# Kernel optimization log

Hardware: AMD Instinct MI355X
Metric: run time of the kernel (lower is better)

The kernel has to match this reference:

```python
import jax, jax.numpy as jnp
import numpy as np

V = 50000   # input_size == output_size (one-hot vocab)
H = 256     # hidden_size
B = 512     # batch_size
L = 1       # num_layers

def setup_inputs() -> dict:
    key = jax.random.key(0)
    ks = jax.random.split(key, 9)
    s = 1.0 / np.sqrt(H)  # torch default uniform(-1/sqrt(H), 1/sqrt(H))
    inp = {
        "input": jax.random.randint(ks[0], (B,), 0, V, dtype=jnp.int64 if jax.config.jax_enable_x64 else jnp.int32),
        "target": jax.random.randint(ks[1], (B,), 0, V, dtype=jnp.int64 if jax.config.jax_enable_x64 else jnp.int32),
        "hidden": jax.random.normal(ks[2], (L, B, H), dtype=jnp.float32),
        "w_ih": jax.random.uniform(ks[3], (3 * H, V), jnp.float32, -s, s),
        "w_hh": jax.random.uniform(ks[4], (3 * H, H), jnp.float32, -s, s),
        "b_ih": jax.random.uniform(ks[5], (3 * H,), jnp.float32, -s, s),
        "b_hh": jax.random.uniform(ks[6], (3 * H,), jnp.float32, -s, s),
        "w_out": jax.random.uniform(ks[7], (V, H), jnp.float32, -s, s),
        "b_out": jax.random.uniform(ks[8], (V,), jnp.float32, -s, s),
    }
    return inp

def reference(input, target, hidden, w_ih, w_hh, b_ih, b_hh, w_out, b_out):
    # one-hot(input) @ w_ih.T is exactly a row-gather from w_ih.T  -> (B, 3H)
    h0 = hidden[0]                              # (B, H), num_layers == 1
    x_proj = w_ih.T[input] + b_ih               # (B, 3H)
    h_proj = h0 @ w_hh.T + b_hh                 # (B, 3H)
    xr, xz, xn = jnp.split(x_proj, 3, axis=-1)
    hr, hz, hn = jnp.split(h_proj, 3, axis=-1)
    r = jax.nn.sigmoid(xr + hr)                 # reset gate
    z = jax.nn.sigmoid(xz + hz)                 # update gate
    n = jnp.tanh(xn + r * hn)                   # candidate
    h1 = (1.0 - z) * n + z * h0                 # (B, H)
    logit = jnp.tanh(h1 @ w_out.T + b_out)      # (B, V)
    return logit, h1[None]                      # (B,V), (1,B,H)
```

## Files before the change

### kernel.cpp

```cpp
#include <hip/hip_runtime.h>
#include <hip/hip_bf16.h>

#define VOCAB 50000
#define HID   256
#define BATCH 512
#define GH    768

typedef __attribute__((ext_vector_type(8))) __bf16 bf16x8;
typedef __attribute__((ext_vector_type(4))) float f32x4;
typedef __attribute__((ext_vector_type(4))) unsigned int u32x4;

union BFrag {
    bf16x8 v;
    u32x4  q;
    __bf16 b[8];
};

__device__ __forceinline__ float fast_sigmoid(float x) {
    return 1.0f / (1.0f + __expf(-x));
}
__device__ __forceinline__ float fast_tanh(float x) {
    return 1.0f - 2.0f / (1.0f + __expf(2.0f * x));
}

__device__ __forceinline__ void cvt8(BFrag& t, f32x4 lo, f32x4 hi) {
    t.b[0] = (__bf16)lo.x; t.b[1] = (__bf16)lo.y;
    t.b[2] = (__bf16)lo.z; t.b[3] = (__bf16)lo.w;
    t.b[4] = (__bf16)hi.x; t.b[5] = (__bf16)hi.y;
    t.b[6] = (__bf16)hi.z; t.b[7] = (__bf16)hi.w;
}

__device__ __forceinline__ void gload_lds16(const void* g, void* l) {
    __builtin_amdgcn_global_load_lds(
        (const __attribute__((address_space(1))) unsigned int*)g,
        (__attribute__((address_space(3))) unsigned int*)l, 16, 0, 0);
}


__global__ __launch_bounds__(256, 4) void gemm_dma(
    const char* __restrict__ Aswz, const float* __restrict__ Bm,
    float* __restrict__ C, const float* __restrict__ bias, int mChunks)
{
    __shared__ char ldsA[2][16384];

    const int tid  = threadIdx.x;
    const int wid  = tid >> 6;
    const int lane = tid & 63;
    const int r    = lane & 15;
    const int g    = lane >> 4;
    const int col  = blockIdx.x * 64 + wid * 16 + r;
    const int bcol = col < VOCAB ? col : (VOCAB - 1);

    BFrag bf[8];
    {
        const f32x4* wrow = reinterpret_cast<const f32x4*>(Bm + (size_t)bcol * 256);
        #pragma unroll
        for (int kk = 0; kk < 8; kk++) {
            f32x4 lo = __builtin_nontemporal_load(&wrow[kk * 8 + g * 2]);
            f32x4 hi = __builtin_nontemporal_load(&wrow[kk * 8 + g * 2 + 1]);
            cvt8(bf[kk], lo, hi);
        }
    }
    #pragma unroll
    for (int kk = 0; kk < 8; kk++)
        asm volatile("" : "+v"(bf[kk].q));
    const float biasv = bias[bcol];

    auto dma = [&](int c, int buf) {
        const char* src = Aswz + (size_t)c * 16384 + wid * 1024 + lane * 16;
        char* dst = &ldsA[buf][wid * 1024];
        #pragma unroll
        for (int i = 0; i < 4; i++)
            gload_lds16(src + i * 4096, dst + i * 4096);
    };

    dma(0, 0);
    asm volatile("s_waitcnt vmcnt(0)" ::: "memory");
    __builtin_amdgcn_s_barrier();

    for (int c = 0; c < mChunks; c++) {
        const int cur = c & 1;
        if (c + 1 < mChunks) dma(c + 1, cur ^ 1);
        __builtin_amdgcn_sched_barrier(0);

        f32x4 acc0 = (f32x4){0.f, 0.f, 0.f, 0.f};
        f32x4 acc1 = (f32x4){0.f, 0.f, 0.f, 0.f};

        #pragma unroll
        for (int kk = 0; kk < 8; kk++) {
            const int s0 = r * 512 + ((((kk << 2) + g) ^ (r & 7)) << 4);
            BFrag a0, a1;
            a0.q = *reinterpret_cast<const u32x4*>(&ldsA[cur][s0]);
            a1.q = *reinterpret_cast<const u32x4*>(&ldsA[cur][s0 + 8192]);
            acc0 = __builtin_amdgcn_mfma_f32_16x16x32_bf16(a0.v, bf[kk].v, acc0, 0, 0, 0);
            acc1 = __builtin_amdgcn_mfma_f32_16x16x32_bf16(a1.v, bf[kk].v, acc1, 0, 0, 0);
        }

        const int rowb = c * 32 + g * 4;
        #pragma unroll
        for (int j = 0; j < 4; j++) {
            float v0 = fast_tanh(acc0[j] + biasv);
            float v1 = fast_tanh(acc1[j] + biasv);
            C[(size_t)(rowb + j) * VOCAB + bcol]      = v0;
            C[(size_t)(rowb + 16 + j) * VOCAB + bcol] = v1;
        }

        if (c + 1 < mChunks) {
            asm volatile("s_waitcnt vmcnt(8)" ::: "memory");
            __builtin_amdgcn_s_barrier();
        }
    }
}

__global__ __launch_bounds__(256, 4) void gemm_h(
    const float* __restrict__ A, const float* __restrict__ Bm,
    float* __restrict__ C)
{
    __shared__ char ldsA[16384];

    const int tid  = threadIdx.x;
    const int wid  = tid >> 6;
    const int lane = tid & 63;
    const int r    = lane & 15;
    const int g    = lane >> 4;
    const int col  = blockIdx.x * 64 + wid * 16 + r;
    const int mbase = blockIdx.y * 32;

    BFrag bf[8];
    {
        const f32x4* wrow = reinterpret_cast<const f32x4*>(Bm + (size_t)col * 256);
        #pragma unroll
        for (int kk = 0; kk < 8; kk++)
            cvt8(bf[kk], wrow[kk * 8 + g * 2], wrow[kk * 8 + g * 2 + 1]);
    }

    {
        const f32x4* src = reinterpret_cast<const f32x4*>(A + (size_t)mbase * 256);
        #pragma unroll
        for (int i = 0; i < 4; i++) {
            int u = tid + i * 256;
            int row = u >> 5, jj = u & 31;
            BFrag t; cvt8(t, src[2 * u], src[2 * u + 1]);
            int byte = row * 512 + ((jj ^ (row & 7)) << 4);
            *reinterpret_cast<u32x4*>(&ldsA[byte]) = t.q;
        }
    }
    __syncthreads();

    f32x4 acc0 = (f32x4){0.f, 0.f, 0.f, 0.f};
    f32x4 acc1 = (f32x4){0.f, 0.f, 0.f, 0.f};
    #pragma unroll
    for (int kk = 0; kk < 8; kk++) {
        const int s0 = r * 512 + ((((kk << 2) + g) ^ (r & 7)) << 4);
        BFrag a0, a1;
        a0.q = *reinterpret_cast<const u32x4*>(&ldsA[s0]);
        a1.q = *reinterpret_cast<const u32x4*>(&ldsA[s0 + 8192]);
        acc0 = __builtin_amdgcn_mfma_f32_16x16x32_bf16(a0.v, bf[kk].v, acc0, 0, 0, 0);
        acc1 = __builtin_amdgcn_mfma_f32_16x16x32_bf16(a1.v, bf[kk].v, acc1, 0, 0, 0);
    }

    const int rowb = mbase + g * 4;
    #pragma unroll
    for (int j = 0; j < 4; j++) {
        C[(size_t)(rowb + j) * GH + col]      = acc0[j];
        C[(size_t)(rowb + 16 + j) * GH + col] = acc1[j];
    }
}

__global__ __launch_bounds__(256) void gru_gate(
    const int* __restrict__ inp, const float* __restrict__ hidden,
    const float* __restrict__ w_ih, const float* __restrict__ b_ih,
    const float* __restrict__ b_hh, const float* __restrict__ hproj,
    float* __restrict__ h1out, char* __restrict__ h1swz)
{
    const int b = blockIdx.x;
    const int k = threadIdx.x;
    const int c = inp[b];

    float xr = w_ih[(size_t)k * VOCAB + c]         + b_ih[k];
    float xz = w_ih[(size_t)(k + 256) * VOCAB + c] + b_ih[k + 256];
    float xn = w_ih[(size_t)(k + 512) * VOCAB + c] + b_ih[k + 512];

    float hr = hproj[b * GH + k]       + b_hh[k];
    float hz = hproj[b * GH + 256 + k] + b_hh[k + 256];
    float hn = hproj[b * GH + 512 + k] + b_hh[k + 512];

    float rg = fast_sigmoid(xr + hr);
    float zg = fast_sigmoid(xz + hz);
    float ng = fast_tanh(xn + rg * hn);
    float h0 = hidden[b * HID + k];
    float h1 = (1.0f - zg) * ng + zg * h0;

    h1out[b * HID + k] = h1;

    const int row = b & 31, j = k >> 3, e = k & 7;
    size_t byte = (size_t)(b >> 5) * 16384 + row * 512
                + ((j ^ (row & 7)) << 4) + e * 2;
    __bf16 hb = (__bf16)h1;
    *reinterpret_cast<unsigned short*>(h1swz + byte) =
        __builtin_bit_cast(unsigned short, hb);
}

extern "C" void kernel_launch(void* const* d_in, const int* in_sizes, int n_in,
                              void* d_out, int out_size, void* d_ws, size_t ws_size,
                              hipStream_t stream) {
    const int*   input  = (const int*)  d_in[0];
    const float* hidden = (const float*)d_in[2];
    const float* w_ih   = (const float*)d_in[3];
    const float* w_hh   = (const float*)d_in[4];
    const float* b_ih   = (const float*)d_in[5];
    const float* b_hh   = (const float*)d_in[6];
    const float* w_out  = (const float*)d_in[7];
    const float* b_out  = (const float*)d_in[8];

    float* logit = (float*)d_out;
    float* h1    = (float*)d_out + (size_t)BATCH * VOCAB;

    char*  h1swz = (char*)d_ws;
    float* hproj = (float*)((char*)d_ws + 256 * 1024);

    dim3 g1(GH / 64, BATCH / 32);
    gemm_h<<<g1, 256, 0, stream>>>(hidden, w_hh, hproj);

    gru_gate<<<BATCH, 256, 0, stream>>>(input, hidden, w_ih, b_ih, b_hh, hproj,
                                        h1, h1swz);

    dim3 g3((VOCAB + 63) / 64, 1);
    gemm_dma<<<g3, 256, 0, stream>>>(h1swz, w_out, logit, b_out, 16);
}
```

Measured before the change: 70.29 us.

## Transpose MFMA operands for vectorized logit stores and register-staged A pipeline

Swaps the MFMA A/B operands so each lane owns four consecutive output columns, enabling 16-byte vector stores and vector bias loads for the large logit matrix. Replaces the direct global-to-LDS DMA staging with register-prefetched loads that are swizzled on write into double-buffered LDS. The gate kernel now emits plain row-major bf16 h1. This targets store coalescing on the write-bound output, at the cost of extra registers and LDS write instructions.

After: 67.48 us. -4.0%, faster.

```diff
diff --git a/kernel.cpp b/kernel.cpp
--- a/kernel.cpp
+++ b/kernel.cpp
@@ -30,15 +30,8 @@
     t.b[6] = (__bf16)hi.z; t.b[7] = (__bf16)hi.w;
 }
 
-__device__ __forceinline__ void gload_lds16(const void* g, void* l) {
-    __builtin_amdgcn_global_load_lds(
-        (const __attribute__((address_space(1))) unsigned int*)g,
-        (__attribute__((address_space(3))) unsigned int*)l, 16, 0, 0);
-}
-
-
-__global__ __launch_bounds__(256, 4) void gemm_dma(
-    const char* __restrict__ Aswz, const float* __restrict__ Bm,
+__global__ __launch_bounds__(256, 4) void gemm_swp(
+    const unsigned short* __restrict__ Abf, const float* __restrict__ Bm,
     float* __restrict__ C, const float* __restrict__ bias, int mChunks)
 {
     __shared__ char ldsA[2][16384];
@@ -48,12 +41,12 @@
     const int lane = tid & 63;
     const int r    = lane & 15;
     const int g    = lane >> 4;
-    const int col  = blockIdx.x * 64 + wid * 16 + r;
-    const int bcol = col < VOCAB ? col : (VOCAB - 1);
+    const int wcol = blockIdx.x * 64 + wid * 16 + r;
+    const int bw   = wcol < VOCAB ? wcol : (VOCAB - 1);
 
     BFrag bf[8];
     {
-        const f32x4* wrow = reinterpret_cast<const f32x4*>(Bm + (size_t)bcol * 256);
+        const f32x4* wrow = reinterpret_cast<const f32x4*>(Bm + (size_t)bw * 256);
         #pragma unroll
         for (int kk = 0; kk < 8; kk++) {
             f32x4 lo = __builtin_nontemporal_load(&wrow[kk * 8 + g * 2]);
@@ -64,24 +57,39 @@
     #pragma unroll
     for (int kk = 0; kk < 8; kk++)
         asm volatile("" : "+v"(bf[kk].q));
-    const float biasv = bias[bcol];
-
-    auto dma = [&](int c, int buf) {
-        const char* src = Aswz + (size_t)c * 16384 + wid * 1024 + lane * 16;
-        char* dst = &ldsA[buf][wid * 1024];
-        #pragma unroll
-        for (int i = 0; i < 4; i++)
-            gload_lds16(src + i * 4096, dst + i * 4096);
+
+    const int vcol0   = blockIdx.x * 64 + wid * 16 + g * 4;
+    const bool storeok = (vcol0 + 3 < VOCAB);
+    const int bvc     = storeok ? vcol0 : (VOCAB - 4);
+    const f32x4 b4    = *reinterpret_cast<const f32x4*>(bias + bvc);
+
+    u32x4 areg[4];
+    auto load_chunk = [&](int c) {
+        const u32x4* src = reinterpret_cast<const u32x4*>(Abf + (size_t)c * 32 * 256);
+        #pragma unroll
+        for (int i = 0; i < 4; i++) areg[i] = src[tid + i * 256];
     };
-
-    dma(0, 0);
-    asm volatile("s_waitcnt vmcnt(0)" ::: "memory");
-    __builtin_amdgcn_s_barrier();
+    auto write_lds = [&](int buf) {
+        #pragma unroll
+        for (int i = 0; i < 4; i++) {
+            int u = tid + i * 256;
+            int row = u >> 5, j = u & 31;
+            int byte = row * 512 + ((j ^ (row & 7)) << 4);
+            *reinterpret_cast<u32x4*>(&ldsA[buf][byte]) = areg[i];
+        }
+    };
+
+    load_chunk(0);
+    write_lds(0);
+    if (mChunks > 1) load_chunk(1);
+    asm volatile("s_waitcnt lgkmcnt(0)\n\ts_barrier" ::: "memory");
 
     for (int c = 0; c < mChunks; c++) {
         const int cur = c & 1;
-        if (c + 1 < mChunks) dma(c + 1, cur ^ 1);
-        __builtin_amdgcn_sched_barrier(0);
+        if (c + 1 < mChunks) {
+            write_lds(cur ^ 1);
+            if (c + 2 < mChunks) load_chunk(c + 2);
+        }
 
         f32x4 acc0 = (f32x4){0.f, 0.f, 0.f, 0.f};
         f32x4 acc1 = (f32x4){0.f, 0.f, 0.f, 0.f};
@@ -92,23 +100,24 @@
             BFrag a0, a1;
             a0.q = *reinterpret_cast<const u32x4*>(&ldsA[cur][s0]);
             a1.q = *reinterpret_cast<const u32x4*>(&ldsA[cur][s0 + 8192]);
-            acc0 = __builtin_amdgcn_mfma_f32_16x16x32_bf16(a0.v, bf[kk].v, acc0, 0, 0, 0);
-            acc1 = __builtin_amdgcn_mfma_f32_16x16x32_bf16(a1.v, bf[kk].v, acc1, 0, 0, 0);
-        }
-
-        const int rowb = c * 32 + g * 4;
-        #pragma unroll
-        for (int j = 0; j < 4; j++) {
-            float v0 = fast_tanh(acc0[j] + biasv);
-            float v1 = fast_tanh(acc1[j] + biasv);
-            C[(size_t)(rowb + j) * VOCAB + bcol]      = v0;
-            C[(size_t)(rowb + 16 + j) * VOCAB + bcol] = v1;
-        }
-
-        if (c + 1 < mChunks) {
-            asm volatile("s_waitcnt vmcnt(8)" ::: "memory");
-            __builtin_amdgcn_s_barrier();
-        }
+            acc0 = __builtin_amdgcn_mfma_f32_16x16x32_bf16(bf[kk].v, a0.v, acc0, 0, 0, 0);
+            acc1 = __builtin_amdgcn_mfma_f32_16x16x32_bf16(bf[kk].v, a1.v, acc1, 0, 0, 0);
+        }
+
+        if (storeok) {
+            const int row0 = c * 32 + r;
+            f32x4 v0, v1;
+            #pragma unroll
+            for (int j = 0; j < 4; j++) {
+                v0[j] = fast_tanh(acc0[j] + b4[j]);
+                v1[j] = fast_tanh(acc1[j] + b4[j]);
+            }
+            *reinterpret_cast<f32x4*>(&C[(size_t)row0 * VOCAB + vcol0])        = v0;
+            *reinterpret_cast<f32x4*>(&C[(size_t)(row0 + 16) * VOCAB + vcol0]) = v1;
+        }
+
+        if (c + 1 < mChunks)
+            asm volatile("s_waitcnt lgkmcnt(0)\n\ts_barrier" ::: "memory");
     }
 }
 
@@ -171,7 +180,7 @@
     const int* __restrict__ inp, const float* __restrict__ hidden,
     const float* __restrict__ w_ih, const float* __restrict__ b_ih,
     const float* __restrict__ b_hh, const float* __restrict__ hproj,
-    float* __restrict__ h1out, char* __restrict__ h1swz)
+    float* __restrict__ h1out, unsigned short* __restrict__ h1bf)
 {
     const int b = blockIdx.x;
     const int k = threadIdx.x;
@@ -192,13 +201,8 @@
     float h1 = (1.0f - zg) * ng + zg * h0;
 
     h1out[b * HID + k] = h1;
-
-    const int row = b & 31, j = k >> 3, e = k & 7;
-    size_t byte = (size_t)(b >> 5) * 16384 + row * 512
-                + ((j ^ (row & 7)) << 4) + e * 2;
     __bf16 hb = (__bf16)h1;
-    *reinterpret_cast<unsigned short*>(h1swz + byte) =
-        __builtin_bit_cast(unsigned short, hb);
+    h1bf[b * HID + k] = __builtin_bit_cast(unsigned short, hb);
 }
 
 extern "C" void kernel_launch(void* const* d_in, const int* in_sizes, int n_in,
@@ -216,15 +220,15 @@
     float* logit = (float*)d_out;
     float* h1    = (float*)d_out + (size_t)BATCH * VOCAB;
 
-    char*  h1swz = (char*)d_ws;
-    float* hproj = (float*)((char*)d_ws + 256 * 1024);
+    float*          hproj = (float*)d_ws;
+    unsigned short* h1bf  = (unsigned short*)((char*)d_ws + (size_t)BATCH * GH * 4);
 
     dim3 g1(GH / 64, BATCH / 32);
     gemm_h<<<g1, 256, 0, stream>>>(hidden, w_hh, hproj);
 
     gru_gate<<<BATCH, 256, 0, stream>>>(input, hidden, w_ih, b_ih, b_hh, hproj,
-                                        h1, h1swz);
+                                        h1, h1bf);
 
     dim3 g3((VOCAB + 63) / 64, 1);
-    gemm_dma<<<g3, 256, 0, stream>>>(h1swz, w_out, logit, b_out, 16);
-}
+    gemm_swp<<<g3, 256, 0, stream>>>(h1bf, w_out, logit, b_out, 16);
+}
```
